# Kernel optimization log

Measured on AMD Instinct MI355X. Metric: run time of the kernel, lower is better.

The kernel has to match this reference:

```python
import jax, jax.numpy as jnp
import numpy as np

N_NODES = 50000
N_EDGES = 600000
IN_DIM = 128
HID = 128
OUT_DIM = 10
N_GRAPHS = 512
LN_EPS = 1e-5
N_CELLS = 4  # len(macro_architecture) + 1


def setup_inputs() -> dict:
    key = jax.random.key(0)
    ks = jax.random.split(key, 8)
    s = 0.05
    x = jax.random.normal(ks[0], (N_NODES, IN_DIM), dtype=jnp.float32)
    edge_index = jax.random.randint(ks[1], (2, N_EDGES), 0, N_NODES, dtype=jnp.int32)
    batch = jnp.sort(jax.random.randint(ks[2], (N_NODES,), 0, N_GRAPHS, dtype=jnp.int32))
    return {
        "x": x,
        "edge_index": edge_index,
        "batch": batch,
        "W_pre": jax.random.normal(ks[3], (IN_DIM, HID), dtype=jnp.float32) * s,
        "b_pre": jnp.zeros((HID,), jnp.float32),
        "conv_W": jax.random.normal(ks[4], (N_CELLS, HID, HID), dtype=jnp.float32) * s,
        "conv_b": jnp.zeros((N_CELLS, HID), jnp.float32),
        "ln_g": jnp.ones((N_CELLS, HID), jnp.float32),
        "ln_b": jnp.zeros((N_CELLS, HID), jnp.float32),
        "W_post": jax.random.normal(ks[5], (HID, OUT_DIM), dtype=jnp.float32) * s,
        "b_post": jnp.zeros((OUT_DIM,), jnp.float32),
    }


def _gcn_conv(x, W, b, src, dst):
    """GCNConv: add self-loops, symmetric deg^-1/2 normalization, gather-scatter."""
    n = x.shape[0]
    h = x @ W                                   # [N, HID]
    loops = jnp.arange(n, dtype=src.dtype)
    s = jnp.concatenate([src, loops])           # [E + N]
    d = jnp.concatenate([dst, loops])
    deg = jax.ops.segment_sum(jnp.ones_like(d, jnp.float32), d, num_segments=n)
    dinv = jax.lax.rsqrt(jnp.maximum(deg, 1.0))  # deg >= 1 via self-loops
    coef = dinv[s] * dinv[d]                    # [E + N]
    out = jax.ops.segment_sum(h[s] * coef[:, None], d, num_segments=n)
    return out + b


def _layer_norm(x, g, b):
    mu = jnp.mean(x, axis=-1, keepdims=True)
    var = jnp.var(x, axis=-1, keepdims=True)
    return (x - mu) * jax.lax.rsqrt(var + LN_EPS) * g + b


def _cell(x, i, conv_W, conv_b, ln_g, ln_b, src, dst):
    h = _gcn_conv(x, conv_W[i], conv_b[i], src, dst)
    return jax.nn.relu(_layer_norm(h, ln_g[i], ln_b[i]))


def reference(x, edge_index, batch, W_pre, b_pre, conv_W, conv_b, ln_g, ln_b, W_post, b_post):
    src, dst = edge_index[0], edge_index[1]
    # pre MLP
    h0 = x @ W_pre + b_pre
    # state node 0 (all 3 outgoing edges active -> identical output reused)
    n0 = _cell(h0, 0, conv_W, conv_b, ln_g, ln_b, src, dst)
    # state node 1: input = node0's output
    n1 = _cell(n0, 1, conv_W, conv_b, ln_g, ln_b, src, dst)
    # second-to-last node: sum of [-2] outputs (n0, n1)
    s2l = _cell(n0 + n1, 2, conv_W, conv_b, ln_g, ln_b, src, dst)
    # last node: sum of [-1] outputs (n0, n1) + second-to-last output
    last = _cell(n0 + n1 + s2l, 3, conv_W, conv_b, ln_g, ln_b, src, dst)
    # sum pooling by graph id, then post MLP
    pooled = jax.ops.segment_sum(last, batch, num_segments=N_GRAPHS)  # [G, HID]
    return pooled @ W_post + b_post
```

## Files before the change

kernel.cpp:

```cpp
#include <hip/hip_runtime.h>

#define HID 128
#define LN_EPS 1e-5f

using f32x4 = __attribute__((ext_vector_type(4))) float;
using s16x8 = __attribute__((ext_vector_type(8))) short;

__device__ inline float bl2f(unsigned u) { u <<= 16; return __builtin_bit_cast(float, u); }
__device__ inline float bh2f(unsigned u) { u &= 0xffff0000u; return __builtin_bit_cast(float, u); }
__device__ inline unsigned f2b_bits(float f) {
  unsigned u = __builtin_bit_cast(unsigned, f);
  return (u + 0x7fffu + ((u >> 16) & 1u)) >> 16;
}
__device__ inline short f2b(float f) { return (short)f2b_bits(f); }
__device__ inline unsigned pack2(float a, float b) { return f2b_bits(a) | (f2b_bits(b) << 16); }

__device__ inline void addu4(const uint4 u, float a[8]) {
  a[0] += bl2f(u.x); a[1] += bh2f(u.x);
  a[2] += bl2f(u.y); a[3] += bh2f(u.y);
  a[4] += bl2f(u.z); a[5] += bh2f(u.z);
  a[6] += bl2f(u.w); a[7] += bh2f(u.w);
}


__global__ __launch_bounds__(128) void prep_comb_kernel(const float* __restrict__ W_pre,
                                                        const float* __restrict__ b_pre,
                                                        const float* __restrict__ convW0,
                                                        float* __restrict__ Wc,
                                                        float* __restrict__ bprime) {
  int m = blockIdx.x;
  int t = threadIdx.x;
  const float* arow = (m == HID) ? b_pre : W_pre + (size_t)m * HID;
  float acc = 0.f;
  #pragma unroll 8
  for (int k = 0; k < HID; ++k) acc = fmaf(arow[k], convW0[(size_t)k * HID + t], acc);
  if (m == HID) bprime[t] = acc;
  else Wc[(size_t)m * HID + t] = acc;
}


__global__ __launch_bounds__(64) void prep_w_kernel(const float* __restrict__ Wc,
                                                    const float* __restrict__ conv_W,
                                                    short* __restrict__ Wt) {
  int b = blockIdx.x;
  int w = b >> 7, n = b & 127;
  const float* W = (w == 0) ? Wc : conv_W + (size_t)w * HID * HID;
  int t = threadIdx.x;
  float f0 = W[(2 * t) * HID + n];
  float f1 = W[(2 * t + 1) * HID + n];
  ((unsigned*)Wt)[(size_t)(w * HID + n) * 64 + t] = pack2(f0, f1);
}


__global__ void zero_ints_kernel(int* __restrict__ p, int n) {
  int i = blockIdx.x * blockDim.x + threadIdx.x;
  if (i < n) p[i] = 0;
}

__global__ void deg_count_kernel(const int* __restrict__ dst, int E, int* __restrict__ deg) {
  int e = blockIdx.x * blockDim.x + threadIdx.x;
  if (e < E) atomicAdd(&deg[dst[e]], 1);
}

__global__ __launch_bounds__(256) void alloc_kernel(const int* __restrict__ deg,
                                                    int* __restrict__ start,
                                                    int* __restrict__ cur,
                                                    float* __restrict__ dinv,
                                                    int* __restrict__ cnt, int n) {
  __shared__ int wt[4];
  __shared__ int bbase;
  int t = threadIdx.x, lane = t & 63, wid = t >> 6;
  int i = blockIdx.x * 256 + t;
  int d = (i < n) ? deg[i] : 0;
  int x = d;
  #pragma unroll
  for (int off = 1; off < 64; off <<= 1) {
    int u = __shfl_up(x, off, 64);
    if (lane >= off) x += u;
  }
  if (lane == 63) wt[wid] = x;
  __syncthreads();
  if (t == 0) bbase = atomicAdd(cnt, wt[0] + wt[1] + wt[2] + wt[3]);
  __syncthreads();
  int wbase = bbase;
  for (int w = 0; w < wid; ++w) wbase += wt[w];
  int excl = wbase + x - d;
  if (i < n) {
    start[i] = excl;
    cur[i] = excl;
    dinv[i] = rsqrtf((float)(d + 1));
  }
}

__global__ void fill_csr_kernel(const int* __restrict__ src, const int* __restrict__ dst,
                                int E, int* __restrict__ cur, int* __restrict__ col) {
  int e = blockIdx.x * blockDim.x + threadIdx.x;
  if (e < E) {
    int d = dst[e];
    int p = atomicAdd(&cur[d], 1);
    col[p] = src[e];
  }
}


template<bool AF32>
__global__ __launch_bounds__(256) void gemm_mfma_kernel(
    const void* __restrict__ Xv, const short* __restrict__ Wt,
    const float* __restrict__ bias, const float* __restrict__ dinv,
    short* __restrict__ Y, int M) {
  __shared__ short lds[4 * 32 * HID];
  int t = threadIdx.x;
  int wave = t >> 6, l = t & 63;
  int lg = l >> 4, lr = l & 15;
  int mb = blockIdx.x * 128 + wave * 32;

  const f32x4 z4 = {0.f, 0.f, 0.f, 0.f};
  f32x4 acc[2][8];
  #pragma unroll
  for (int i = 0; i < 2; ++i)
    #pragma unroll
    for (int j = 0; j < 8; ++j) acc[i][j] = z4;

  const short* Xb = (const short*)Xv;
  const float* Xf = (const float*)Xv;

  #pragma unroll
  for (int kk = 0; kk < 4; ++kk) {
    int k0 = kk * 32 + lg * 8;
    s16x8 a[2];
    #pragma unroll
    for (int mf = 0; mf < 2; ++mf) {
      int row = mb + mf * 16 + lr;
      s16x8 av = {0, 0, 0, 0, 0, 0, 0, 0};
      if (row < M) {
        if constexpr (AF32) {
          const float4* p = (const float4*)(Xf + (size_t)row * HID + k0);
          float4 x0 = p[0], x1 = p[1];
          av[0] = f2b(x0.x); av[1] = f2b(x0.y); av[2] = f2b(x0.z); av[3] = f2b(x0.w);
          av[4] = f2b(x1.x); av[5] = f2b(x1.y); av[6] = f2b(x1.z); av[7] = f2b(x1.w);
        } else {
          av = *(const s16x8*)(Xb + (size_t)row * HID + k0);
        }
      }
      a[mf] = av;
    }
    #pragma unroll
    for (int nf = 0; nf < 8; ++nf) {
      s16x8 b = *(const s16x8*)(Wt + (size_t)(nf * 16 + lr) * HID + k0);
      acc[0][nf] = __builtin_amdgcn_mfma_f32_16x16x32_bf16(a[0], b, acc[0][nf], 0, 0, 0);
      acc[1][nf] = __builtin_amdgcn_mfma_f32_16x16x32_bf16(a[1], b, acc[1][nf], 0, 0, 0);
    }
  }

  float bv[8];
  #pragma unroll
  for (int nf = 0; nf < 8; ++nf) bv[nf] = bias ? bias[nf * 16 + lr] : 0.f;

  short* wsl = lds + wave * 32 * HID;
  #pragma unroll
  for (int mf = 0; mf < 2; ++mf) {
    #pragma unroll
    for (int r = 0; r < 4; ++r) {
      int ri = mf * 16 + lg * 4 + r;
      int row = mb + ri;
      float dv = 1.f;
      if (dinv && row < M) dv = dinv[row];
      #pragma unroll
      for (int nf = 0; nf < 8; ++nf) {
        float v = (acc[mf][nf][r] + bv[nf]) * dv;
        wsl[ri * HID + nf * 16 + lr] = f2b(v);
      }
    }
  }
  __syncthreads();

  #pragma unroll
  for (int it = 0; it < 8; ++it) {
    int ro = it * 4 + lg;
    int row = mb + ro;
    s16x8 v = *(const s16x8*)(wsl + it * 512 + l * 8);
    if (row < M) *(s16x8*)(Y + (size_t)row * HID + lr * 8) = v;
  }
}


__global__ __launch_bounds__(256) void agg_ln_kernel(
    const short* __restrict__ G, const int* __restrict__ start, const int* __restrict__ deg,
    const float* __restrict__ dinv, const float* __restrict__ bias,
    const float* __restrict__ lng, const float* __restrict__ lnb,
    const int* __restrict__ col,
    short* __restrict__ y, short* __restrict__ accum, int N, int mode) {
  int wave = threadIdx.x >> 6, l = threadIdx.x & 63;
  int v = blockIdx.x * 4 + wave;
  if (v >= N) return;
  int lr = l & 15, sub = l >> 4;

  const uint4* GR = (const uint4*)G;
  float a[8] = {0.f, 0.f, 0.f, 0.f, 0.f, 0.f, 0.f, 0.f};

  if (sub == 0) addu4(GR[(size_t)v * 16 + lr], a);

  int lo = start[v], hi = lo + deg[v];
  int j = lo;
  for (; j + 8 <= hi; j += 8) {
    int c0 = col[j + sub];
    int c1 = col[j + 4 + sub];
    uint4 u0 = GR[(size_t)c0 * 16 + lr];
    uint4 u1 = GR[(size_t)c1 * 16 + lr];
    addu4(u0, a);
    addu4(u1, a);
  }
  for (; j < hi; j += 4) {
    if (j + sub < hi) addu4(GR[(size_t)col[j + sub] * 16 + lr], a);
  }

  #pragma unroll
  for (int i = 0; i < 8; ++i) {
    a[i] += __shfl_xor(a[i], 16, 64);
    a[i] += __shfl_xor(a[i], 32, 64);
  }

  float d = dinv[v];
  const float4* bp4 = (const float4*)(bias + 8 * lr);
  float4 bc0 = bp4[0], bc1 = bp4[1];
  float bb[8] = {bc0.x, bc0.y, bc0.z, bc0.w, bc1.x, bc1.y, bc1.z, bc1.w};
  #pragma unroll
  for (int i = 0; i < 8; ++i) a[i] = fmaf(a[i], d, bb[i]);

  float s1 = 0.f, s2 = 0.f;
  #pragma unroll
  for (int i = 0; i < 8; ++i) { s1 += a[i]; s2 = fmaf(a[i], a[i], s2); }
  #pragma unroll
  for (int off = 1; off <= 8; off <<= 1) {
    s1 += __shfl_xor(s1, off, 64);
    s2 += __shfl_xor(s2, off, 64);
  }
  float mu = s1 * (1.f / HID);
  float var = s2 * (1.f / HID) - mu * mu;
  float inv = rsqrtf(fmaxf(var, 0.f) + LN_EPS);

  const float4* gp4 = (const float4*)(lng + 8 * lr);
  const float4* pp4 = (const float4*)(lnb + 8 * lr);
  float4 g0 = gp4[0], g1 = gp4[1], p0 = pp4[0], p1 = pp4[1];
  float gg[8] = {g0.x, g0.y, g0.z, g0.w, g1.x, g1.y, g1.z, g1.w};
  float pb[8] = {p0.x, p0.y, p0.z, p0.w, p1.x, p1.y, p1.z, p1.w};
  float yv[8];
  #pragma unroll
  for (int i = 0; i < 8; ++i) yv[i] = fmaxf(fmaf((a[i] - mu) * inv, gg[i], pb[i]), 0.f);

  if (sub == 0) {
    uint4 o;
    o.x = pack2(yv[0], yv[1]); o.y = pack2(yv[2], yv[3]);
    o.z = pack2(yv[4], yv[5]); o.w = pack2(yv[6], yv[7]);
    uint4* Yw = (uint4*)y;
    uint4* Aw = (uint4*)accum;
    size_t idx = (size_t)v * 16 + lr;
    if (mode == 0) { Yw[idx] = o; Aw[idx] = o; }
    else if (mode == 1) {
      uint4 po = Aw[idx];
      uint4 q;
      q.x = pack2(bl2f(po.x) + yv[0], bh2f(po.x) + yv[1]);
      q.y = pack2(bl2f(po.y) + yv[2], bh2f(po.y) + yv[3]);
      q.z = pack2(bl2f(po.z) + yv[4], bh2f(po.z) + yv[5]);
      q.w = pack2(bl2f(po.w) + yv[6], bh2f(po.w) + yv[7]);
      Aw[idx] = q;
    } else {
      Yw[idx] = o;
    }
  }
}


__device__ inline int lower_bound_i(const int* a, int n, int key) {
  int lo = 0, hi = n;
  while (lo < hi) { int m = (lo + hi) >> 1; if (a[m] < key) lo = m + 1; else hi = m; }
  return lo;
}

__global__ __launch_bounds__(128) void pool_post_kernel(
    const short* __restrict__ Yl, const int* __restrict__ batch, int n,
    const float* __restrict__ Wp, const float* __restrict__ bp,
    float* __restrict__ out, int n_out) {
  int g = blockIdx.x, t = threadIdx.x;
  int wave = t >> 6;
  int lr = t & 15, slot = t >> 4;
  int lo = lower_bound_i(batch, n, g);
  int hi = lower_bound_i(batch, n, g + 1);
  const uint4* YR = (const uint4*)Yl;
  float a[8] = {0.f, 0.f, 0.f, 0.f, 0.f, 0.f, 0.f, 0.f};
  for (int r = lo + slot; r < hi; r += 8) addu4(YR[(size_t)r * 16 + lr], a);
  #pragma unroll
  for (int i = 0; i < 8; ++i) {
    a[i] += __shfl_xor(a[i], 16, 64);
    a[i] += __shfl_xor(a[i], 32, 64);
  }
  __shared__ float ls[2][HID];
  if ((slot & 3) == 0) {
    #pragma unroll
    for (int i = 0; i < 8; ++i) ls[wave][8 * lr + i] = a[i];
  }
  __syncthreads();
  if (t < n_out) {
    float o = bp[t];
    #pragma unroll 8
    for (int k = 0; k < HID; ++k) o = fmaf(ls[0][k] + ls[1][k], Wp[k * n_out + t], o);
    out[g * n_out + t] = o;
  }
}


extern "C" void kernel_launch(void* const* d_in, const int* in_sizes, int n_in,
                              void* d_out, int out_size, void* d_ws, size_t ws_size,
                              hipStream_t stream) {
  const float* x      = (const float*)d_in[0];
  const int*   ei     = (const int*)d_in[1];
  const int*   batch  = (const int*)d_in[2];
  const float* W_pre  = (const float*)d_in[3];
  const float* b_pre  = (const float*)d_in[4];
  const float* conv_W = (const float*)d_in[5];
  const float* conv_b = (const float*)d_in[6];
  const float* ln_g   = (const float*)d_in[7];
  const float* ln_b   = (const float*)d_in[8];
  const float* W_post = (const float*)d_in[9];
  const float* b_post = (const float*)d_in[10];
  float* out = (float*)d_out;

  const int N = in_sizes[2];
  const int E = in_sizes[1] / 2;
  const int OUT_DIM = 10;
  const int NG = out_size / OUT_DIM;

  char* p = (char*)d_ws;
  short* ACC = (short*)p;            p += (size_t)N * HID * 2;
  short* B1  = (short*)p;            p += (size_t)N * HID * 2;
  short* G   = (short*)p;            p += (size_t)N * HID * 2;
  short* Wt  = (short*)p;            p += (size_t)4 * HID * HID * 2;
  float* Wc  = (float*)p;            p += (size_t)HID * HID * 4;
  float* bpr = (float*)p;            p += (size_t)HID * 4;
  float* dinv = (float*)p;           p += (size_t)N * 4;
  int* deg   = (int*)p;              p += (size_t)(N + 1) * 4;
  int* startv = (int*)p;             p += (size_t)N * 4;
  int* cur   = (int*)p;              p += (size_t)N * 4;
  int* col   = (int*)p;              p += (size_t)E * 4;
  int* cnt   = deg + N;

  const int* srcp = ei;
  const int* dstp = ei + E;

  int nb256 = (N + 255) / 256;
  int eb256 = (E + 255) / 256;
  int gemm_grid = (N + 127) / 128;
  int agg_grid = (N + 3) / 4;

  prep_comb_kernel<<<HID + 1, HID, 0, stream>>>(W_pre, b_pre, conv_W, Wc, bpr);
  prep_w_kernel<<<4 * HID, 64, 0, stream>>>(Wc, conv_W, Wt);

  zero_ints_kernel<<<nb256, 256, 0, stream>>>(deg, N + 1);
  deg_count_kernel<<<eb256, 256, 0, stream>>>(dstp, E, deg);
  alloc_kernel<<<nb256, 256, 0, stream>>>(deg, startv, cur, dinv, cnt, N);
  fill_csr_kernel<<<eb256, 256, 0, stream>>>(srcp, dstp, E, cur, col);

  gemm_mfma_kernel<true><<<gemm_grid, 256, 0, stream>>>(x, Wt + 0 * 16384, bpr, dinv, G, N);
  agg_ln_kernel<<<agg_grid, 256, 0, stream>>>(G, startv, deg, dinv, conv_b + 0 * HID,
                                              ln_g + 0 * HID, ln_b + 0 * HID, col, B1, ACC, N, 0);
  gemm_mfma_kernel<false><<<gemm_grid, 256, 0, stream>>>(B1, Wt + 1 * 16384, nullptr, dinv, G, N);
  agg_ln_kernel<<<agg_grid, 256, 0, stream>>>(G, startv, deg, dinv, conv_b + 1 * HID,
                                              ln_g + 1 * HID, ln_b + 1 * HID, col, nullptr, ACC, N, 1);
  gemm_mfma_kernel<false><<<gemm_grid, 256, 0, stream>>>(ACC, Wt + 2 * 16384, nullptr, dinv, G, N);
  agg_ln_kernel<<<agg_grid, 256, 0, stream>>>(G, startv, deg, dinv, conv_b + 2 * HID,
                                              ln_g + 2 * HID, ln_b + 2 * HID, col, nullptr, ACC, N, 1);
  gemm_mfma_kernel<false><<<gemm_grid, 256, 0, stream>>>(ACC, Wt + 3 * 16384, nullptr, dinv, G, N);
  agg_ln_kernel<<<agg_grid, 256, 0, stream>>>(G, startv, deg, dinv, conv_b + 3 * HID,
                                              ln_g + 3 * HID, ln_b + 3 * HID, col, B1, nullptr, N, 2);

  pool_post_kernel<<<NG, 128, 0, stream>>>(B1, batch, N, W_post, b_post, out, OUT_DIM);
}
```

Baseline: 301.5 us.

## Fuse GCN aggregation+LayerNorm with the next layer's MFMA GEMM

Adds a kernel that aggregates neighbours, applies LayerNorm/ReLU and the residual accumulation for a 64-row tile, stages the result in swizzled LDS, then multiplies by the next layer's weight with bf16 MFMA and writes the scaled output. This removes three separate GEMM launches and the global write/read of the intermediate activations between them. In exchange each block does 16 sequential gather rows per wave before the GEMM, so there is less parallelism for latency hiding. The weight B fragments are read directly from global memory.

```diff
diff --git a/kernel.cpp b/kernel.cpp
--- a/kernel.cpp
+++ b/kernel.cpp
@@ -184,12 +184,143 @@
 }
 
 
+__global__ __launch_bounds__(256) void agg_ln_gemm_kernel(
+    const short* __restrict__ G_in, const int* __restrict__ start,
+    const int* __restrict__ deg, const float* __restrict__ dinv,
+    const float* __restrict__ bias, const float* __restrict__ lng,
+    const float* __restrict__ lnb, const int* __restrict__ col,
+    short* __restrict__ ACC, const short* __restrict__ Wt,
+    short* __restrict__ G_out, int N, int mode) {
+  __shared__ short As[64 * HID];
+  int t = threadIdx.x;
+  int wave = t >> 6, l = t & 63, lr = l & 15, sub = l >> 4;
+  const uint4* GR = (const uint4*)G_in;
+  uint4* Aw = (uint4*)ACC;
+
+  const float4* bp4 = (const float4*)(bias + 8 * lr);
+  const float4* gp4 = (const float4*)(lng + 8 * lr);
+  const float4* pp4 = (const float4*)(lnb + 8 * lr);
+  float4 bc0 = bp4[0], bc1 = bp4[1];
+  float4 g0 = gp4[0], g1 = gp4[1];
+  float4 p0 = pp4[0], p1 = pp4[1];
+  float bb[8] = {bc0.x, bc0.y, bc0.z, bc0.w, bc1.x, bc1.y, bc1.z, bc1.w};
+  float gg[8] = {g0.x, g0.y, g0.z, g0.w, g1.x, g1.y, g1.z, g1.w};
+  float pb[8] = {p0.x, p0.y, p0.z, p0.w, p1.x, p1.y, p1.z, p1.w};
+
+  for (int s = 0; s < 16; ++s) {
+    int rowL = wave * 16 + s;
+    int v = blockIdx.x * 64 + rowL;
+    int lidx = rowL * HID + ((lr * 8) ^ ((rowL & 7) << 3));
+    if (v >= N) {
+      if (sub == 0) *(uint4*)&As[lidx] = make_uint4(0, 0, 0, 0);
+      continue;
+    }
+    float a[8] = {0.f, 0.f, 0.f, 0.f, 0.f, 0.f, 0.f, 0.f};
+    if (sub == 0) addu4(GR[(size_t)v * 16 + lr], a);
+    int lo = start[v], hi = lo + deg[v];
+    int j = lo;
+    for (; j + 8 <= hi; j += 8) {
+      int c0 = col[j + sub];
+      int c1 = col[j + 4 + sub];
+      uint4 u0 = GR[(size_t)c0 * 16 + lr];
+      uint4 u1 = GR[(size_t)c1 * 16 + lr];
+      addu4(u0, a);
+      addu4(u1, a);
+    }
+    for (; j < hi; j += 4)
+      if (j + sub < hi) addu4(GR[(size_t)col[j + sub] * 16 + lr], a);
+
+    #pragma unroll
+    for (int i = 0; i < 8; ++i) {
+      a[i] += __shfl_xor(a[i], 16, 64);
+      a[i] += __shfl_xor(a[i], 32, 64);
+    }
+
+    float d = dinv[v];
+    #pragma unroll
+    for (int i = 0; i < 8; ++i) a[i] = fmaf(a[i], d, bb[i]);
+
+    float s1 = 0.f, s2 = 0.f;
+    #pragma unroll
+    for (int i = 0; i < 8; ++i) { s1 += a[i]; s2 = fmaf(a[i], a[i], s2); }
+    #pragma unroll
+    for (int off = 1; off <= 8; off <<= 1) {
+      s1 += __shfl_xor(s1, off, 64);
+      s2 += __shfl_xor(s2, off, 64);
+    }
+    float mu = s1 * (1.f / HID);
+    float var = s2 * (1.f / HID) - mu * mu;
+    float inv = rsqrtf(fmaxf(var, 0.f) + LN_EPS);
+
+    float yv[8];
+    #pragma unroll
+    for (int i = 0; i < 8; ++i) yv[i] = fmaxf(fmaf((a[i] - mu) * inv, gg[i], pb[i]), 0.f);
+
+    if (sub == 0) {
+      size_t idx = (size_t)v * 16 + lr;
+      uint4 q;
+      if (mode == 0) {
+        q.x = pack2(yv[0], yv[1]); q.y = pack2(yv[2], yv[3]);
+        q.z = pack2(yv[4], yv[5]); q.w = pack2(yv[6], yv[7]);
+      } else {
+        uint4 po = Aw[idx];
+        q.x = pack2(bl2f(po.x) + yv[0], bh2f(po.x) + yv[1]);
+        q.y = pack2(bl2f(po.y) + yv[2], bh2f(po.y) + yv[3]);
+        q.z = pack2(bl2f(po.z) + yv[4], bh2f(po.z) + yv[5]);
+        q.w = pack2(bl2f(po.w) + yv[6], bh2f(po.w) + yv[7]);
+      }
+      Aw[idx] = q;
+      *(uint4*)&As[lidx] = q;
+    }
+  }
+
+  int lg = sub;
+  const f32x4 z4 = {0.f, 0.f, 0.f, 0.f};
+  f32x4 acc[8];
+  #pragma unroll
+  for (int j = 0; j < 8; ++j) acc[j] = z4;
+
+  #pragma unroll
+  for (int kk = 0; kk < 4; ++kk) {
+    int k0 = kk * 32 + lg * 8;
+    int rowA = wave * 16 + lr;
+    s16x8 af = *(const s16x8*)&As[rowA * HID + (k0 ^ ((rowA & 7) << 3))];
+    #pragma unroll
+    for (int nf = 0; nf < 8; ++nf) {
+      s16x8 b = *(const s16x8*)(Wt + (size_t)(nf * 16 + lr) * HID + k0);
+      acc[nf] = __builtin_amdgcn_mfma_f32_16x16x32_bf16(af, b, acc[nf], 0, 0, 0);
+    }
+  }
+
+  short* wsl = As + wave * 16 * HID;
+  float dv[4];
+  #pragma unroll
+  for (int r = 0; r < 4; ++r) {
+    int row = blockIdx.x * 64 + wave * 16 + lg * 4 + r;
+    dv[r] = (row < N) ? dinv[row] : 1.f;
+  }
+  #pragma unroll
+  for (int r = 0; r < 4; ++r) {
+    int ri = lg * 4 + r;
+    #pragma unroll
+    for (int nf = 0; nf < 8; ++nf)
+      wsl[ri * HID + nf * 16 + lr] = f2b(acc[nf][r] * dv[r]);
+  }
+  #pragma unroll
+  for (int it = 0; it < 4; ++it) {
+    int rl = it * 4 + sub;
+    int row = blockIdx.x * 64 + wave * 16 + rl;
+    s16x8 vv = *(const s16x8*)(wsl + rl * HID + lr * 8);
+    if (row < N) *(s16x8*)(G_out + (size_t)row * HID + lr * 8) = vv;
+  }
+}
+
+
 __global__ __launch_bounds__(256) void agg_ln_kernel(
     const short* __restrict__ G, const int* __restrict__ start, const int* __restrict__ deg,
     const float* __restrict__ dinv, const float* __restrict__ bias,
     const float* __restrict__ lng, const float* __restrict__ lnb,
-    const int* __restrict__ col,
-    short* __restrict__ y, short* __restrict__ accum, int N, int mode) {
+    const int* __restrict__ col, short* __restrict__ y, int N) {
   int wave = threadIdx.x >> 6, l = threadIdx.x & 63;
   int v = blockIdx.x * 4 + wave;
   if (v >= N) return;
@@ -210,9 +341,8 @@
     addu4(u0, a);
     addu4(u1, a);
   }
-  for (; j < hi; j += 4) {
+  for (; j < hi; j += 4)
     if (j + sub < hi) addu4(GR[(size_t)col[j + sub] * 16 + lr], a);
-  }
 
   #pragma unroll
   for (int i = 0; i < 8; ++i) {
@@ -252,21 +382,7 @@
     uint4 o;
     o.x = pack2(yv[0], yv[1]); o.y = pack2(yv[2], yv[3]);
     o.z = pack2(yv[4], yv[5]); o.w = pack2(yv[6], yv[7]);
-    uint4* Yw = (uint4*)y;
-    uint4* Aw = (uint4*)accum;
-    size_t idx = (size_t)v * 16 + lr;
-    if (mode == 0) { Yw[idx] = o; Aw[idx] = o; }
-    else if (mode == 1) {
-      uint4 po = Aw[idx];
-      uint4 q;
-      q.x = pack2(bl2f(po.x) + yv[0], bh2f(po.x) + yv[1]);
-      q.y = pack2(bl2f(po.y) + yv[2], bh2f(po.y) + yv[3]);
-      q.z = pack2(bl2f(po.z) + yv[4], bh2f(po.z) + yv[5]);
-      q.w = pack2(bl2f(po.w) + yv[6], bh2f(po.w) + yv[7]);
-      Aw[idx] = q;
-    } else {
-      Yw[idx] = o;
-    }
+    ((uint4*)y)[(size_t)v * 16 + lr] = o;
   }
 }
 
@@ -332,8 +448,8 @@
 
   char* p = (char*)d_ws;
   short* ACC = (short*)p;            p += (size_t)N * HID * 2;
-  short* B1  = (short*)p;            p += (size_t)N * HID * 2;
-  short* G   = (short*)p;            p += (size_t)N * HID * 2;
+  short* G0  = (short*)p;            p += (size_t)N * HID * 2;
+  short* G1  = (short*)p;            p += (size_t)N * HID * 2;
   short* Wt  = (short*)p;            p += (size_t)4 * HID * HID * 2;
   float* Wc  = (float*)p;            p += (size_t)HID * HID * 4;
   float* bpr = (float*)p;            p += (size_t)HID * 4;
@@ -350,6 +466,7 @@
   int nb256 = (N + 255) / 256;
   int eb256 = (E + 255) / 256;
   int gemm_grid = (N + 127) / 128;
+  int fused_grid = (N + 63) / 64;
   int agg_grid = (N + 3) / 4;
 
   prep_comb_kernel<<<HID + 1, HID, 0, stream>>>(W_pre, b_pre, conv_W, Wc, bpr);
@@ -360,18 +477,19 @@
   alloc_kernel<<<nb256, 256, 0, stream>>>(deg, startv, cur, dinv, cnt, N);
   fill_csr_kernel<<<eb256, 256, 0, stream>>>(srcp, dstp, E, cur, col);
 
-  gemm_mfma_kernel<true><<<gemm_grid, 256, 0, stream>>>(x, Wt + 0 * 16384, bpr, dinv, G, N);
-  agg_ln_kernel<<<agg_grid, 256, 0, stream>>>(G, startv, deg, dinv, conv_b + 0 * HID,
-                                              ln_g + 0 * HID, ln_b + 0 * HID, col, B1, ACC, N, 0);
-  gemm_mfma_kernel<false><<<gemm_grid, 256, 0, stream>>>(B1, Wt + 1 * 16384, nullptr, dinv, G, N);
-  agg_ln_kernel<<<agg_grid, 256, 0, stream>>>(G, startv, deg, dinv, conv_b + 1 * HID,
-                                              ln_g + 1 * HID, ln_b + 1 * HID, col, nullptr, ACC, N, 1);
-  gemm_mfma_kernel<false><<<gemm_grid, 256, 0, stream>>>(ACC, Wt + 2 * 16384, nullptr, dinv, G, N);
-  agg_ln_kernel<<<agg_grid, 256, 0, stream>>>(G, startv, deg, dinv, conv_b + 2 * HID,
-                                              ln_g + 2 * HID, ln_b + 2 * HID, col, nullptr, ACC, N, 1);
-  gemm_mfma_kernel<false><<<gemm_grid, 256, 0, stream>>>(ACC, Wt + 3 * 16384, nullptr, dinv, G, N);
-  agg_ln_kernel<<<agg_grid, 256, 0, stream>>>(G, startv, deg, dinv, conv_b + 3 * HID,
-                                              ln_g + 3 * HID, ln_b + 3 * HID, col, B1, nullptr, N, 2);
-
-  pool_post_kernel<<<NG, 128, 0, stream>>>(B1, batch, N, W_post, b_post, out, OUT_DIM);
-}
+  gemm_mfma_kernel<true><<<gemm_grid, 256, 0, stream>>>(x, Wt + 0 * 16384, bpr, dinv, G0, N);
+
+  agg_ln_gemm_kernel<<<fused_grid, 256, 0, stream>>>(G0, startv, deg, dinv, conv_b + 0 * HID,
+                                                     ln_g + 0 * HID, ln_b + 0 * HID, col,
+                                                     ACC, Wt + 1 * 16384, G1, N, 0);
+  agg_ln_gemm_kernel<<<fused_grid, 256, 0, stream>>>(G1, startv, deg, dinv, conv_b + 1 * HID,
+                                                     ln_g + 1 * HID, ln_b + 1 * HID, col,
+                                                     ACC, Wt + 2 * 16384, G0, N, 1);
+  agg_ln_gemm_kernel<<<fused_grid, 256, 0, stream>>>(G0, startv, deg, dinv, conv_b + 2 * HID,
+                                                     ln_g + 2 * HID, ln_b + 2 * HID, col,
+                                                     ACC, Wt + 3 * 16384, G1, N, 1);
+  agg_ln_kernel<<<agg_grid, 256, 0, stream>>>(G1, startv, deg, dinv, conv_b + 3 * HID,
+                                              ln_g + 3 * HID, ln_b + 3 * HID, col, G0, N);
+
+  pool_post_kernel<<<NG, 128, 0, stream>>>(G0, batch, N, W_post, b_post, out, OUT_DIM);
+}
```

Measured after the change: 344.1 us. +14.1%, slower.

## Fuse gather, GEMM and LayerNorm per cell by aggregating before the transform

Applied to the files above, without the earlier changes.

The GCN order is switched from transform-then-aggregate to aggregate-then-transform: each cell kernel gathers dinv-scaled neighbour rows into LDS, multiplies the 16-row tile by the cell weight with MFMA, then applies bias, LayerNorm and ReLU and writes the dinv-prescaled running sum. This removes the three separate per-cell GEMM launches and the intermediate G buffer round trip through global memory. The precomputed W_pre·W0 combination is dropped, so the pre-MLP GEMM writes directly into the first cell's input. The cost is a small 16-row MFMA tile per block with weights read from global memory each time, plus extra block-level syncs.

```diff
diff --git a/kernel.cpp b/kernel.cpp
--- a/kernel.cpp
+++ b/kernel.cpp
@@ -8,6 +8,10 @@
 
 __device__ inline float bl2f(unsigned u) { u <<= 16; return __builtin_bit_cast(float, u); }
 __device__ inline float bh2f(unsigned u) { u &= 0xffff0000u; return __builtin_bit_cast(float, u); }
+__device__ inline float sb2f(short s) {
+  unsigned u = ((unsigned)(unsigned short)s) << 16;
+  return __builtin_bit_cast(float, u);
+}
 __device__ inline unsigned f2b_bits(float f) {
   unsigned u = __builtin_bit_cast(unsigned, f);
   return (u + 0x7fffu + ((u >> 16) & 1u)) >> 16;
@@ -23,28 +27,12 @@
 }
 
 
-__global__ __launch_bounds__(128) void prep_comb_kernel(const float* __restrict__ W_pre,
-                                                        const float* __restrict__ b_pre,
-                                                        const float* __restrict__ convW0,
-                                                        float* __restrict__ Wc,
-                                                        float* __restrict__ bprime) {
-  int m = blockIdx.x;
-  int t = threadIdx.x;
-  const float* arow = (m == HID) ? b_pre : W_pre + (size_t)m * HID;
-  float acc = 0.f;
-  #pragma unroll 8
-  for (int k = 0; k < HID; ++k) acc = fmaf(arow[k], convW0[(size_t)k * HID + t], acc);
-  if (m == HID) bprime[t] = acc;
-  else Wc[(size_t)m * HID + t] = acc;
-}
-
-
-__global__ __launch_bounds__(64) void prep_w_kernel(const float* __restrict__ Wc,
+__global__ __launch_bounds__(64) void prep_w_kernel(const float* __restrict__ W_pre,
                                                     const float* __restrict__ conv_W,
                                                     short* __restrict__ Wt) {
   int b = blockIdx.x;
   int w = b >> 7, n = b & 127;
-  const float* W = (w == 0) ? Wc : conv_W + (size_t)w * HID * HID;
+  const float* W = (w == 0) ? W_pre : conv_W + (size_t)(w - 1) * HID * HID;
   int t = threadIdx.x;
   float f0 = W[(2 * t) * HID + n];
   float f1 = W[(2 * t + 1) * HID + n];
@@ -184,88 +172,137 @@
 }
 
 
-__global__ __launch_bounds__(256) void agg_ln_kernel(
-    const short* __restrict__ G, const int* __restrict__ start, const int* __restrict__ deg,
-    const float* __restrict__ dinv, const float* __restrict__ bias,
-    const float* __restrict__ lng, const float* __restrict__ lnb,
-    const int* __restrict__ col,
-    short* __restrict__ y, short* __restrict__ accum, int N, int mode) {
-  int wave = threadIdx.x >> 6, l = threadIdx.x & 63;
-  int v = blockIdx.x * 4 + wave;
-  if (v >= N) return;
-  int lr = l & 15, sub = l >> 4;
-
-  const uint4* GR = (const uint4*)G;
-  float a[8] = {0.f, 0.f, 0.f, 0.f, 0.f, 0.f, 0.f, 0.f};
-
-  if (sub == 0) addu4(GR[(size_t)v * 16 + lr], a);
-
-  int lo = start[v], hi = lo + deg[v];
-  int j = lo;
-  for (; j + 8 <= hi; j += 8) {
-    int c0 = col[j + sub];
-    int c1 = col[j + 4 + sub];
-    uint4 u0 = GR[(size_t)c0 * 16 + lr];
-    uint4 u1 = GR[(size_t)c1 * 16 + lr];
-    addu4(u0, a);
-    addu4(u1, a);
-  }
-  for (; j < hi; j += 4) {
-    if (j + sub < hi) addu4(GR[(size_t)col[j + sub] * 16 + lr], a);
-  }
-
-  #pragma unroll
-  for (int i = 0; i < 8; ++i) {
-    a[i] += __shfl_xor(a[i], 16, 64);
-    a[i] += __shfl_xor(a[i], 32, 64);
-  }
-
-  float d = dinv[v];
-  const float4* bp4 = (const float4*)(bias + 8 * lr);
-  float4 bc0 = bp4[0], bc1 = bp4[1];
-  float bb[8] = {bc0.x, bc0.y, bc0.z, bc0.w, bc1.x, bc1.y, bc1.z, bc1.w};
-  #pragma unroll
-  for (int i = 0; i < 8; ++i) a[i] = fmaf(a[i], d, bb[i]);
-
-  float s1 = 0.f, s2 = 0.f;
-  #pragma unroll
-  for (int i = 0; i < 8; ++i) { s1 += a[i]; s2 = fmaf(a[i], a[i], s2); }
+__global__ __launch_bounds__(512) void cell_kernel(
+    const short* __restrict__ Sin, const int* __restrict__ start,
+    const int* __restrict__ deg, const float* __restrict__ dinv,
+    const int* __restrict__ col, const short* __restrict__ Wt,
+    const float* __restrict__ bconv, const float* __restrict__ lng,
+    const float* __restrict__ lnb, short* __restrict__ Sout,
+    int N, int mode) {
+  __shared__ short Zs[16 * HID];
+  __shared__ float red[16][8][2];
+  int t = threadIdx.x;
+  int wave = t >> 6, l = t & 63, lr = l & 15, sub = l >> 4;
+  int lg = sub;
+  const uint4* GR = (const uint4*)Sin;
+
+  #pragma unroll
+  for (int s2 = 0; s2 < 2; ++s2) {
+    int rowL = wave * 2 + s2;
+    int v = blockIdx.x * 16 + rowL;
+    int zofs = rowL * HID + ((lr * 8) ^ ((rowL & 7) << 3));
+    if (v >= N) {
+      if (sub == 0) *(uint4*)&Zs[zofs] = make_uint4(0u, 0u, 0u, 0u);
+      continue;
+    }
+    float a[8] = {0.f, 0.f, 0.f, 0.f, 0.f, 0.f, 0.f, 0.f};
+    if (sub == 0) addu4(GR[(size_t)v * 16 + lr], a);
+    int lo = start[v], hi = lo + deg[v];
+    int j = lo;
+    for (; j + 8 <= hi; j += 8) {
+      int c0 = col[j + sub];
+      int c1 = col[j + 4 + sub];
+      uint4 u0 = GR[(size_t)c0 * 16 + lr];
+      uint4 u1 = GR[(size_t)c1 * 16 + lr];
+      addu4(u0, a);
+      addu4(u1, a);
+    }
+    for (; j < hi; j += 4)
+      if (j + sub < hi) addu4(GR[(size_t)col[j + sub] * 16 + lr], a);
+
+    #pragma unroll
+    for (int i = 0; i < 8; ++i) {
+      a[i] += __shfl_xor(a[i], 16, 64);
+      a[i] += __shfl_xor(a[i], 32, 64);
+    }
+    float d = dinv[v];
+    if (sub == 0) {
+      uint4 q;
+      q.x = pack2(a[0] * d, a[1] * d); q.y = pack2(a[2] * d, a[3] * d);
+      q.z = pack2(a[4] * d, a[5] * d); q.w = pack2(a[6] * d, a[7] * d);
+      *(uint4*)&Zs[zofs] = q;
+    }
+  }
+  __syncthreads();
+
+  f32x4 acc = {0.f, 0.f, 0.f, 0.f};
+  #pragma unroll
+  for (int kk = 0; kk < 4; ++kk) {
+    int k0 = kk * 32 + lg * 8;
+    s16x8 af = *(const s16x8*)&Zs[lr * HID + (k0 ^ ((lr & 7) << 3))];
+    s16x8 bf = *(const s16x8*)(Wt + (size_t)(wave * 16 + lr) * HID + k0);
+    acc = __builtin_amdgcn_mfma_f32_16x16x32_bf16(af, bf, acc, 0, 0, 0);
+  }
+  int c = wave * 16 + lr;
+  float bc = bconv[c];
+  float h[4], s1[4], s2v[4];
+  #pragma unroll
+  for (int r = 0; r < 4; ++r) {
+    h[r] = acc[r] + bc;
+    s1[r] = h[r];
+    s2v[r] = h[r] * h[r];
+  }
   #pragma unroll
   for (int off = 1; off <= 8; off <<= 1) {
-    s1 += __shfl_xor(s1, off, 64);
-    s2 += __shfl_xor(s2, off, 64);
-  }
-  float mu = s1 * (1.f / HID);
-  float var = s2 * (1.f / HID) - mu * mu;
-  float inv = rsqrtf(fmaxf(var, 0.f) + LN_EPS);
-
-  const float4* gp4 = (const float4*)(lng + 8 * lr);
-  const float4* pp4 = (const float4*)(lnb + 8 * lr);
-  float4 g0 = gp4[0], g1 = gp4[1], p0 = pp4[0], p1 = pp4[1];
-  float gg[8] = {g0.x, g0.y, g0.z, g0.w, g1.x, g1.y, g1.z, g1.w};
-  float pb[8] = {p0.x, p0.y, p0.z, p0.w, p1.x, p1.y, p1.z, p1.w};
-  float yv[8];
-  #pragma unroll
-  for (int i = 0; i < 8; ++i) yv[i] = fmaxf(fmaf((a[i] - mu) * inv, gg[i], pb[i]), 0.f);
-
-  if (sub == 0) {
-    uint4 o;
-    o.x = pack2(yv[0], yv[1]); o.y = pack2(yv[2], yv[3]);
-    o.z = pack2(yv[4], yv[5]); o.w = pack2(yv[6], yv[7]);
-    uint4* Yw = (uint4*)y;
-    uint4* Aw = (uint4*)accum;
-    size_t idx = (size_t)v * 16 + lr;
-    if (mode == 0) { Yw[idx] = o; Aw[idx] = o; }
-    else if (mode == 1) {
-      uint4 po = Aw[idx];
-      uint4 q;
-      q.x = pack2(bl2f(po.x) + yv[0], bh2f(po.x) + yv[1]);
-      q.y = pack2(bl2f(po.y) + yv[2], bh2f(po.y) + yv[3]);
-      q.z = pack2(bl2f(po.z) + yv[4], bh2f(po.z) + yv[5]);
-      q.w = pack2(bl2f(po.w) + yv[6], bh2f(po.w) + yv[7]);
-      Aw[idx] = q;
-    } else {
-      Yw[idx] = o;
+    #pragma unroll
+    for (int r = 0; r < 4; ++r) {
+      s1[r] += __shfl_xor(s1[r], off, 64);
+      s2v[r] += __shfl_xor(s2v[r], off, 64);
+    }
+  }
+  if (lr == 0) {
+    #pragma unroll
+    for (int r = 0; r < 4; ++r) {
+      red[lg * 4 + r][wave][0] = s1[r];
+      red[lg * 4 + r][wave][1] = s2v[r];
+    }
+  }
+  __syncthreads();
+  float gl = lng[c], bl = lnb[c];
+  #pragma unroll
+  for (int r = 0; r < 4; ++r) {
+    int row = lg * 4 + r;
+    const float4* rp = (const float4*)&red[row][0][0];
+    float t1 = 0.f, t2 = 0.f;
+    #pragma unroll
+    for (int q4 = 0; q4 < 4; ++q4) {
+      float4 vv = rp[q4];
+      t1 += vv.x + vv.z;
+      t2 += vv.y + vv.w;
+    }
+    float mu = t1 * (1.f / HID);
+    float var = t2 * (1.f / HID) - mu * mu;
+    float inv = rsqrtf(fmaxf(var, 0.f) + LN_EPS);
+    float yv = fmaxf(fmaf((h[r] - mu) * inv, gl, bl), 0.f);
+    Zs[row * HID + (c ^ ((row & 7) << 3))] = f2b(yv);
+  }
+  __syncthreads();
+
+  if (t < 256) {
+    int row = t >> 4, q = t & 15;
+    int v = blockIdx.x * 16 + row;
+    if (v < N) {
+      s16x8 y8 = *(const s16x8*)&Zs[row * HID + ((q * 8) ^ ((row & 7) << 3))];
+      float yv[8];
+      #pragma unroll
+      for (int i = 0; i < 8; ++i) yv[i] = sb2f(y8[i]);
+      uint4 o;
+      if (mode == 2) {
+        o.x = pack2(yv[0], yv[1]); o.y = pack2(yv[2], yv[3]);
+        o.z = pack2(yv[4], yv[5]); o.w = pack2(yv[6], yv[7]);
+      } else if (mode == 0) {
+        float d = dinv[v];
+        o.x = pack2(yv[0] * d, yv[1] * d); o.y = pack2(yv[2] * d, yv[3] * d);
+        o.z = pack2(yv[4] * d, yv[5] * d); o.w = pack2(yv[6] * d, yv[7] * d);
+      } else {
+        float d = dinv[v];
+        uint4 ui = GR[(size_t)v * 16 + q];
+        o.x = pack2(bl2f(ui.x) + yv[0] * d, bh2f(ui.x) + yv[1] * d);
+        o.y = pack2(bl2f(ui.y) + yv[2] * d, bh2f(ui.y) + yv[3] * d);
+        o.z = pack2(bl2f(ui.z) + yv[4] * d, bh2f(ui.z) + yv[5] * d);
+        o.w = pack2(bl2f(ui.w) + yv[6] * d, bh2f(ui.w) + yv[7] * d);
+      }
+      ((uint4*)Sout)[(size_t)v * 16 + q] = o;
     }
   }
 }
@@ -331,12 +368,9 @@
   const int NG = out_size / OUT_DIM;
 
   char* p = (char*)d_ws;
-  short* ACC = (short*)p;            p += (size_t)N * HID * 2;
-  short* B1  = (short*)p;            p += (size_t)N * HID * 2;
-  short* G   = (short*)p;            p += (size_t)N * HID * 2;
-  short* Wt  = (short*)p;            p += (size_t)4 * HID * HID * 2;
-  float* Wc  = (float*)p;            p += (size_t)HID * HID * 4;
-  float* bpr = (float*)p;            p += (size_t)HID * 4;
+  short* SA  = (short*)p;            p += (size_t)N * HID * 2;
+  short* SB  = (short*)p;            p += (size_t)N * HID * 2;
+  short* Wt  = (short*)p;            p += (size_t)5 * HID * HID * 2;
   float* dinv = (float*)p;           p += (size_t)N * 4;
   int* deg   = (int*)p;              p += (size_t)(N + 1) * 4;
   int* startv = (int*)p;             p += (size_t)N * 4;
@@ -350,28 +384,29 @@
   int nb256 = (N + 255) / 256;
   int eb256 = (E + 255) / 256;
   int gemm_grid = (N + 127) / 128;
-  int agg_grid = (N + 3) / 4;
-
-  prep_comb_kernel<<<HID + 1, HID, 0, stream>>>(W_pre, b_pre, conv_W, Wc, bpr);
-  prep_w_kernel<<<4 * HID, 64, 0, stream>>>(Wc, conv_W, Wt);
+  int cell_grid = (N + 15) / 16;
+
+  prep_w_kernel<<<5 * HID, 64, 0, stream>>>(W_pre, conv_W, Wt);
 
   zero_ints_kernel<<<nb256, 256, 0, stream>>>(deg, N + 1);
   deg_count_kernel<<<eb256, 256, 0, stream>>>(dstp, E, deg);
   alloc_kernel<<<nb256, 256, 0, stream>>>(deg, startv, cur, dinv, cnt, N);
   fill_csr_kernel<<<eb256, 256, 0, stream>>>(srcp, dstp, E, cur, col);
 
-  gemm_mfma_kernel<true><<<gemm_grid, 256, 0, stream>>>(x, Wt + 0 * 16384, bpr, dinv, G, N);
-  agg_ln_kernel<<<agg_grid, 256, 0, stream>>>(G, startv, deg, dinv, conv_b + 0 * HID,
-                                              ln_g + 0 * HID, ln_b + 0 * HID, col, B1, ACC, N, 0);
-  gemm_mfma_kernel<false><<<gemm_grid, 256, 0, stream>>>(B1, Wt + 1 * 16384, nullptr, dinv, G, N);
-  agg_ln_kernel<<<agg_grid, 256, 0, stream>>>(G, startv, deg, dinv, conv_b + 1 * HID,
-                                              ln_g + 1 * HID, ln_b + 1 * HID, col, nullptr, ACC, N, 1);
-  gemm_mfma_kernel<false><<<gemm_grid, 256, 0, stream>>>(ACC, Wt + 2 * 16384, nullptr, dinv, G, N);
-  agg_ln_kernel<<<agg_grid, 256, 0, stream>>>(G, startv, deg, dinv, conv_b + 2 * HID,
-                                              ln_g + 2 * HID, ln_b + 2 * HID, col, nullptr, ACC, N, 1);
-  gemm_mfma_kernel<false><<<gemm_grid, 256, 0, stream>>>(ACC, Wt + 3 * 16384, nullptr, dinv, G, N);
-  agg_ln_kernel<<<agg_grid, 256, 0, stream>>>(G, startv, deg, dinv, conv_b + 3 * HID,
-                                              ln_g + 3 * HID, ln_b + 3 * HID, col, B1, nullptr, N, 2);
-
-  pool_post_kernel<<<NG, 128, 0, stream>>>(B1, batch, N, W_post, b_post, out, OUT_DIM);
-}
+  gemm_mfma_kernel<true><<<gemm_grid, 256, 0, stream>>>(x, Wt + 0 * 16384, b_pre, dinv, SA, N);
+
+  cell_kernel<<<cell_grid, 512, 0, stream>>>(SA, startv, deg, dinv, col, Wt + 1 * 16384,
+                                             conv_b + 0 * HID, ln_g + 0 * HID, ln_b + 0 * HID,
+                                             SB, N, 0);
+  cell_kernel<<<cell_grid, 512, 0, stream>>>(SB, startv, deg, dinv, col, Wt + 2 * 16384,
+                                             conv_b + 1 * HID, ln_g + 1 * HID, ln_b + 1 * HID,
+                                             SA, N, 1);
+  cell_kernel<<<cell_grid, 512, 0, stream>>>(SA, startv, deg, dinv, col, Wt + 3 * 16384,
+                                             conv_b + 2 * HID, ln_g + 2 * HID, ln_b + 2 * HID,
+                                             SB, N, 1);
+  cell_kernel<<<cell_grid, 512, 0, stream>>>(SB, startv, deg, dinv, col, Wt + 4 * 16384,
+                                             conv_b + 3 * HID, ln_g + 3 * HID, ln_b + 3 * HID,
+                                             SA, N, 2);
+
+  pool_post_kernel<<<NG, 128, 0, stream>>>(SA, batch, N, W_post, b_post, out, OUT_DIM);
+}
```

New measurement: 298.3 us. No clear change (-1.1%).
